# Performance work log

Measured on AMD Instinct MI355X. Metric: run time of the kernel, lower is better.

The kernel has to match this reference:

```python
import jax, jax.numpy as jnp
import numpy as np

N, E, CLIP, HID, H, P, MD, B = 4096, 16384, 512, 1024, 4, 4, 512, 32
OUT2 = P * MD  # 2048


def prelu(x, a):
    return jnp.where(x >= 0, x, a * x)


def add_self_loops(src, dst, edge_attr, n):
    # PyG fill_value='mean': self-loop edge_attr = mean of incoming edge attrs
    sums = jax.ops.segment_sum(edge_attr, dst, num_segments=n)
    cnt = jax.ops.segment_sum(jnp.ones((dst.shape[0], 1), edge_attr.dtype), dst, num_segments=n)
    loop_attr = sums / jnp.maximum(cnt, 1.0)
    idx = jnp.arange(n)
    return (jnp.concatenate([src, idx]), jnp.concatenate([dst, idx]),
            jnp.concatenate([edge_attr, loop_attr], axis=0))


def gat_conv(x, src, dst, edge_attr, W, asrc, adst, We, ae, bias, heads, c):
    # PyG GATConv, concat=False (mean over heads), edge_dim used only in attention
    n = x.shape[0]
    src, dst, edge_attr = add_self_loops(src, dst, edge_attr, n)
    h = (x @ W).reshape(n, heads, c)                      # [N,H,C]
    e = (edge_attr @ We).reshape(-1, heads, c)            # [E',H,C]
    a_s = jnp.einsum('nhc,hc->nh', h, asrc)
    a_d = jnp.einsum('nhc,hc->nh', h, adst)
    a_e = jnp.einsum('ehc,hc->eh', e, ae)
    alpha = jax.nn.leaky_relu(a_s[src] + a_d[dst] + a_e, 0.2)  # [E',H]
    amax = jax.ops.segment_max(alpha, dst, num_segments=n)
    ex = jnp.exp(alpha - amax[dst])
    denom = jax.ops.segment_sum(ex, dst, num_segments=n)
    w = ex / jnp.maximum(denom[dst], 1e-16)
    msg = h[src] * w[:, :, None]                          # [E',H,C]
    out = jax.ops.segment_sum(msg, dst, num_segments=n)   # [N,H,C]
    return out.mean(axis=1) + bias


def attentional_pool(x, batch, gW1, gb1, gp1, gW2, gb2, gp2, gW3, gb3, n_graphs):
    gate = prelu(x @ gW1 + gb1, gp1)
    gate = prelu(gate @ gW2 + gb2, gp2)
    gate = gate @ gW3 + gb3                               # [N,1]
    gmax = jax.ops.segment_max(gate, batch, num_segments=n_graphs)
    ex = jnp.exp(gate - gmax[batch])
    denom = jax.ops.segment_sum(ex, batch, num_segments=n_graphs)
    s = ex / jnp.maximum(denom[batch], 1e-16)             # [N,1]
    return jax.ops.segment_sum(s * x, batch, num_segments=n_graphs)  # [B,F]


def setup_inputs() -> dict:
    key = jax.random.key(0)
    ks = jax.random.split(key, 24)
    sc = 0.05
    inp = {
        'x': jax.random.normal(ks[0], (N, CLIP), jnp.float32),
        'edge_index': jax.random.randint(ks[1], (2, E), 0, N),
        'edge_attr': jax.random.normal(ks[2], (E, CLIP), jnp.float32),
        'batch': jnp.sort(jax.random.randint(ks[3], (N,), 0, B)),
        # GATConv 1
        'W1': jax.random.normal(ks[4], (CLIP, H * HID), jnp.float32) * sc,
        'asrc1': jax.random.normal(ks[5], (H, HID), jnp.float32) * sc,
        'adst1': jax.random.normal(ks[6], (H, HID), jnp.float32) * sc,
        'We1': jax.random.normal(ks[7], (CLIP, H * HID), jnp.float32) * sc,
        'ae1': jax.random.normal(ks[8], (H, HID), jnp.float32) * sc,
        'b1': jnp.zeros((HID,), jnp.float32),
        'p1': jnp.float32(0.25),
        # GATConv 2
        'W2': jax.random.normal(ks[9], (HID, H * OUT2), jnp.float32) * sc,
        'asrc2': jax.random.normal(ks[10], (H, OUT2), jnp.float32) * sc,
        'adst2': jax.random.normal(ks[11], (H, OUT2), jnp.float32) * sc,
        'We2': jax.random.normal(ks[12], (CLIP, H * OUT2), jnp.float32) * sc,
        'ae2': jax.random.normal(ks[13], (H, OUT2), jnp.float32) * sc,
        'b2': jnp.zeros((OUT2,), jnp.float32),
        'p2': jnp.float32(0.25),
        # AttentionalAggregation gate_nn
        'gW1': jax.random.normal(ks[14], (OUT2, HID), jnp.float32) * sc,
        'gb1': jnp.zeros((HID,), jnp.float32),
        'gp1': jnp.float32(0.25),
        'gW2': jax.random.normal(ks[15], (HID, HID), jnp.float32) * sc,
        'gb2': jnp.zeros((HID,), jnp.float32),
        'gp2': jnp.float32(0.25),
        'gW3': jax.random.normal(ks[16], (HID, 1), jnp.float32) * sc,
        'gb3': jnp.zeros((1,), jnp.float32),
    }
    return inp


def reference(x, edge_index, edge_attr, batch,
              W1, asrc1, adst1, We1, ae1, b1, p1,
              W2, asrc2, adst2, We2, ae2, b2, p2,
              gW1, gb1, gp1, gW2, gb2, gp2, gW3, gb3):
    src, dst = edge_index[0], edge_index[1]
    h = gat_conv(x, src, dst, edge_attr, W1, asrc1, adst1, We1, ae1, b1, H, HID)
    h = prelu(h, p1)
    h = gat_conv(h, src, dst, edge_attr, W2, asrc2, adst2, We2, ae2, b2, H, OUT2)
    h = prelu(h, p2)
    pooled = attentional_pool(h, batch, gW1, gb1, gp1, gW2, gb2, gp2, gW3, gb3, B)
    return pooled.reshape(-1, P, MD)  # [B, prefix_length, mbart_dim]
```

## Files before the change

kernel.cpp:

```cpp
#include <hip/hip_runtime.h>
#include <hip/hip_bf16.h>
#include <math.h>

#define N_NODES 4096
#define N_EDGES 16384
#define CLIPD   512
#define HID     1024
#define NH      4
#define OUTD    2048
#define NB      32

typedef __bf16 bf16_t;
typedef bf16_t bf16x8 __attribute__((ext_vector_type(8)));
typedef float f32x4 __attribute__((ext_vector_type(4)));

static __device__ __forceinline__ float lrelu(float x) { return x >= 0.f ? x : 0.2f * x; }

static __device__ __forceinline__ unsigned short f2bf(float f) {
  union { float f; unsigned int u; } v; v.f = f;
  unsigned int u = v.u;
  unsigned int r = (u + 0x7FFFu + ((u >> 16) & 1u)) >> 16;
  return (unsigned short)r;
}
static __device__ __forceinline__ float bf2f(unsigned short u) {
  union { unsigned int i; float f; } v; v.i = ((unsigned int)u) << 16; return v.f;
}

#define GLDS(g, l) __builtin_amdgcn_global_load_lds( \
    (const __attribute__((address_space(1))) void*)(g), \
    (__attribute__((address_space(3))) void*)(l), 16, 0, 0)

__global__ __launch_bounds__(256) void cvt_kernel(const float* __restrict__ in,
                                                  unsigned short* __restrict__ out, int n4) {
  int i = blockIdx.x * 256 + threadIdx.x;
  if (i < n4) {
    float4 f = ((const float4*)in)[i];
    ushort4 o;
    o.x = f2bf(f.x); o.y = f2bf(f.y); o.z = f2bf(f.z); o.w = f2bf(f.w);
    ((ushort4*)out)[i] = o;
  }
}

__global__ __launch_bounds__(256) void tcvt_kernel(const float* __restrict__ in,
                                                   unsigned short* __restrict__ out,
                                                   int K, int N) {
  __shared__ float t[32][33];
  const int k0 = blockIdx.y * 32, n0 = blockIdx.x * 32;
  const int tx = threadIdx.x, ty = threadIdx.y;
#pragma unroll
  for (int i = 0; i < 4; ++i) t[ty + 8 * i][tx] = in[(size_t)(k0 + ty + 8 * i) * N + n0 + tx];
  __syncthreads();
#pragma unroll
  for (int i = 0; i < 4; ++i) out[(size_t)(n0 + ty + 8 * i) * K + k0 + tx] = f2bf(t[tx][ty + 8 * i]);
}

template<int K1, int N1>
__global__ __launch_bounds__(256) void stack_tcvt_kernel(const float* __restrict__ in,
                                                         unsigned short* __restrict__ out,
                                                         float scale) {
  __shared__ float t[32][33];
  const int h = blockIdx.z;
  const int k0 = blockIdx.y * 32, n0 = blockIdx.x * 32;
  const int tx = threadIdx.x, ty = threadIdx.y;
#pragma unroll
  for (int i = 0; i < 4; ++i)
    t[ty + 8 * i][tx] = in[(size_t)(k0 + ty + 8 * i) * (NH * N1) + h * N1 + n0 + tx];
  __syncthreads();
#pragma unroll
  for (int i = 0; i < 4; ++i)
    out[(size_t)(n0 + ty + 8 * i) * (NH * K1) + h * K1 + k0 + tx] = f2bf(scale * t[tx][ty + 8 * i]);
}

template<int C>
__global__ __launch_bounds__(256) void v_kernel(const float* __restrict__ W,
                                                const float* __restrict__ a,
                                                float* __restrict__ v) {
  const int k = blockIdx.x;
  const int tid = threadIdx.x;
  const float* row = W + (size_t)k * (NH * C);
  float acc[NH] = {0.f, 0.f, 0.f, 0.f};
  for (int c = tid; c < C; c += 256) {
    for (int h = 0; h < NH; ++h) acc[h] += row[h * C + c] * a[h * C + c];
  }
  for (int h = 0; h < NH; ++h)
    for (int o = 32; o > 0; o >>= 1) acc[h] += __shfl_down(acc[h], o);
  __shared__ float red[4][NH];
  const int wid = tid >> 6, lane = tid & 63;
  if (lane == 0)
    for (int h = 0; h < NH; ++h) red[wid][h] = acc[h];
  __syncthreads();
  if (tid < NH) v[k * NH + tid] = red[0][tid] + red[1][tid] + red[2][tid] + red[3][tid];
}

template<int C>
__global__ __launch_bounds__(256) void v2_kernel(const float* __restrict__ W,
                                                 const float* __restrict__ a1v,
                                                 const float* __restrict__ a2v,
                                                 float* __restrict__ o1, float* __restrict__ o2) {
  const int k = blockIdx.x;
  const int tid = threadIdx.x;
  const float* row = W + (size_t)k * (NH * C);
  float x1[NH] = {0.f, 0.f, 0.f, 0.f}, x2[NH] = {0.f, 0.f, 0.f, 0.f};
  for (int c = tid; c < C; c += 256) {
    for (int h = 0; h < NH; ++h) {
      float w = row[h * C + c];
      x1[h] += w * a1v[h * C + c];
      x2[h] += w * a2v[h * C + c];
    }
  }
  for (int h = 0; h < NH; ++h)
    for (int o = 32; o > 0; o >>= 1) {
      x1[h] += __shfl_down(x1[h], o);
      x2[h] += __shfl_down(x2[h], o);
    }
  __shared__ float r1[4][NH], r2[4][NH];
  const int wid = tid >> 6, lane = tid & 63;
  if (lane == 0)
    for (int h = 0; h < NH; ++h) { r1[wid][h] = x1[h]; r2[wid][h] = x2[h]; }
  __syncthreads();
  if (tid < NH) o1[k * NH + tid] = r1[0][tid] + r1[1][tid] + r1[2][tid] + r1[3][tid];
  else if (tid < 2 * NH) {
    int h = tid - NH;
    o2[k * NH + h] = r2[0][h] + r2[1][h] + r2[2][h] + r2[3][h];
  }
}

__global__ void deg_kernel(const int* __restrict__ ei, int* __restrict__ deg) {
  int e = blockIdx.x * 256 + threadIdx.x;
  if (e < N_EDGES) atomicAdd(&deg[ei[N_EDGES + e]], 1);
}

__global__ __launch_bounds__(1024) void scan_kernel(const int* __restrict__ deg, int* __restrict__ offs) {
  __shared__ int s[1024];
  const int t = threadIdx.x;
  int d0 = deg[4 * t], d1 = deg[4 * t + 1], d2 = deg[4 * t + 2], d3 = deg[4 * t + 3];
  s[t] = d0 + d1 + d2 + d3;
  __syncthreads();
  for (int off = 1; off < 1024; off <<= 1) {
    int v = (t >= off) ? s[t - off] : 0;
    __syncthreads();
    s[t] += v;
    __syncthreads();
  }
  int base = (t > 0) ? s[t - 1] : 0;
  offs[4 * t] = base;
  offs[4 * t + 1] = base + d0;
  offs[4 * t + 2] = base + d0 + d1;
  offs[4 * t + 3] = base + d0 + d1 + d2;
  if (t == 1023) offs[4096] = s[1023];
}

__global__ void fill_kernel(const int* __restrict__ ei, const int* __restrict__ offs,
                            int* __restrict__ cursor, int* __restrict__ csr_src,
                            int* __restrict__ csr_eid) {
  int e = blockIdx.x * 256 + threadIdx.x;
  if (e >= N_EDGES) return;
  int dst = ei[N_EDGES + e];
  int pos = offs[dst] + atomicAdd(&cursor[dst], 1);
  csr_src[pos] = ei[e];
  csr_eid[pos] = e;
}

__global__ __launch_bounds__(256) void ae_kernel(const float* __restrict__ ea, const int* __restrict__ ei,
                                                 const float* __restrict__ v1, const float* __restrict__ v2,
                                                 float* __restrict__ ae1, float* __restrict__ ae2,
                                                 float* __restrict__ aesum1, float* __restrict__ aesum2) {
  __shared__ float4 v1s[CLIPD];
  __shared__ float4 v2s[CLIPD];
  const int tid = threadIdx.x;
  v1s[tid] = ((const float4*)v1)[tid];
  v1s[tid + 256] = ((const float4*)v1)[tid + 256];
  v2s[tid] = ((const float4*)v2)[tid];
  v2s[tid + 256] = ((const float4*)v2)[tid + 256];
  __syncthreads();
  const int wid = tid >> 6, lane = tid & 63;
  for (int i = 0; i < 16; ++i) {
    const int e = blockIdx.x * 64 + wid * 16 + i;
    const float* row = ea + (size_t)e * CLIPD;
    float a1[NH] = {0.f, 0.f, 0.f, 0.f}, a2[NH] = {0.f, 0.f, 0.f, 0.f};
    for (int k = lane; k < CLIPD; k += 64) {
      float x = row[k];
      float4 w1 = v1s[k];
      float4 w2 = v2s[k];
      a1[0] += x * w1.x; a1[1] += x * w1.y; a1[2] += x * w1.z; a1[3] += x * w1.w;
      a2[0] += x * w2.x; a2[1] += x * w2.y; a2[2] += x * w2.z; a2[3] += x * w2.w;
    }
    for (int h = 0; h < NH; ++h)
      for (int o = 32; o > 0; o >>= 1) {
        a1[h] += __shfl_down(a1[h], o);
        a2[h] += __shfl_down(a2[h], o);
      }
    if (lane == 0) {
      int dst = ei[N_EDGES + e];
      for (int h = 0; h < NH; ++h) {
        ae1[e * NH + h] = a1[h];
        ae2[e * NH + h] = a2[h];
        atomicAdd(&aesum1[dst * NH + h], a1[h]);
        atomicAdd(&aesum2[dst * NH + h], a2[h]);
      }
    }
  }
}

__global__ void loopdiv_kernel(float* __restrict__ s1, float* __restrict__ s2,
                               const int* __restrict__ deg) {
  int i = blockIdx.x * 256 + threadIdx.x;
  if (i >= N_NODES * NH) return;
  float c = fmaxf((float)deg[i >> 2], 1.0f);
  s1[i] /= c;
  s2[i] /= c;
}

__global__ __launch_bounds__(256) void rowdot_x(const float* __restrict__ x,
                                                const float* __restrict__ us, const float* __restrict__ ud,
                                                float* __restrict__ as_, float* __restrict__ ad_) {
  __shared__ float4 su[CLIPD], sd[CLIPD];
  const int tid = threadIdx.x;
  for (int k = tid; k < CLIPD; k += 256) {
    su[k] = ((const float4*)us)[k];
    sd[k] = ((const float4*)ud)[k];
  }
  __syncthreads();
  const int wid = tid >> 6, lane = tid & 63;
  const int n = blockIdx.x * 4 + wid;
  const float* row = x + (size_t)n * CLIPD;
  float s[NH] = {0.f, 0.f, 0.f, 0.f}, d[NH] = {0.f, 0.f, 0.f, 0.f};
  for (int k = lane; k < CLIPD; k += 64) {
    float xv = row[k];
    float4 u = su[k], v = sd[k];
    s[0] += xv * u.x; s[1] += xv * u.y; s[2] += xv * u.z; s[3] += xv * u.w;
    d[0] += xv * v.x; d[1] += xv * v.y; d[2] += xv * v.z; d[3] += xv * v.w;
  }
#pragma unroll
  for (int h = 0; h < NH; ++h)
    for (int o = 32; o > 0; o >>= 1) {
      s[h] += __shfl_down(s[h], o);
      d[h] += __shfl_down(d[h], o);
    }
  if (lane == 0)
    for (int h = 0; h < NH; ++h) {
      as_[n * NH + h] = s[h];
      ad_[n * NH + h] = d[h];
    }
}

__global__ __launch_bounds__(256) void rowdot_o(const unsigned short* __restrict__ rows,
                                                const float* __restrict__ us, const float* __restrict__ ud,
                                                float* __restrict__ as_, float* __restrict__ ad_) {
  __shared__ float4 su[HID], sd[HID];
  const int tid = threadIdx.x;
  for (int k = tid; k < HID; k += 256) {
    su[k] = ((const float4*)us)[k];
    sd[k] = ((const float4*)ud)[k];
  }
  __syncthreads();
  const int wid = tid >> 6, lane = tid & 63;
  const int n = blockIdx.x * 4 + wid;
  const unsigned short* row = rows + (size_t)n * HID;
  float s[NH] = {0.f, 0.f, 0.f, 0.f}, d[NH] = {0.f, 0.f, 0.f, 0.f};
  for (int k2 = lane; k2 < HID / 2; k2 += 64) {
    ushort2 uv = ((const ushort2*)row)[k2];
    float f0 = bf2f(uv.x), f1 = bf2f(uv.y);
    float4 u0 = su[2 * k2], u1 = su[2 * k2 + 1];
    float4 v0 = sd[2 * k2], v1 = sd[2 * k2 + 1];
    s[0] += f0 * u0.x + f1 * u1.x; s[1] += f0 * u0.y + f1 * u1.y;
    s[2] += f0 * u0.z + f1 * u1.z; s[3] += f0 * u0.w + f1 * u1.w;
    d[0] += f0 * v0.x + f1 * v1.x; d[1] += f0 * v0.y + f1 * v1.y;
    d[2] += f0 * v0.z + f1 * v1.z; d[3] += f0 * v0.w + f1 * v1.w;
  }
#pragma unroll
  for (int h = 0; h < NH; ++h)
    for (int o = 32; o > 0; o >>= 1) {
      s[h] += __shfl_down(s[h], o);
      d[h] += __shfl_down(d[h], o);
    }
  if (lane == 0)
    for (int h = 0; h < NH; ++h) {
      as_[n * NH + h] = s[h];
      ad_[n * NH + h] = d[h];
    }
}

template<int C>
__global__ __launch_bounds__(256) void aggn_kernel(const unsigned short* __restrict__ src,
                                                   const float* __restrict__ as_, const float* __restrict__ ad_,
                                                   const float* __restrict__ aee, const float* __restrict__ aeloop,
                                                   const int* __restrict__ offs, const int* __restrict__ csr_src,
                                                   const int* __restrict__ csr_eid,
                                                   unsigned short* __restrict__ out) {
  constexpr int CPT = C / 256;
  const int n = blockIdx.x;
  const int tid = threadIdx.x;
  const int off = offs[n];
  const int deg = offs[n + 1] - off;
  __shared__ float minv[NH], dinv[NH], wself[NH];
  __shared__ float wch[32][NH];
  __shared__ int sch[32];
  if (tid < 64) {
    const int h = tid >> 4, slot = tid & 15;
    const float adn = ad_[n * NH + h];
    const float aself = lrelu(as_[n * NH + h] + adn + aeloop[n * NH + h]);
    float m = (slot == 0) ? aself : -3.0e38f;
    for (int i = slot; i < deg; i += 16) {
      float a = lrelu(as_[csr_src[off + i] * NH + h] + adn + aee[csr_eid[off + i] * NH + h]);
      m = fmaxf(m, a);
    }
    for (int o = 1; o < 16; o <<= 1) m = fmaxf(m, __shfl_xor(m, o));
    float den = (slot == 0) ? __expf(aself - m) : 0.f;
    for (int i = slot; i < deg; i += 16) {
      float a = lrelu(as_[csr_src[off + i] * NH + h] + adn + aee[csr_eid[off + i] * NH + h]);
      den += __expf(a - m);
    }
    for (int o = 1; o < 16; o <<= 1) den += __shfl_xor(den, o);
    if (slot == 0) {
      minv[h] = m;
      dinv[h] = 1.0f / den;
      wself[h] = __expf(aself - m) / den;
    }
  }
  __syncthreads();
  float acc[NH][CPT];
#pragma unroll
  for (int h = 0; h < NH; ++h)
#pragma unroll
    for (int c = 0; c < CPT; ++c) acc[h][c] = 0.f;
  for (int base = 0; base < deg; base += 32) {
    const int cnt = min(32, deg - base);
    if (tid < cnt * NH) {
      const int i = tid >> 2, h = tid & 3;
      const int sidx = csr_src[off + base + i];
      float a = lrelu(as_[sidx * NH + h] + ad_[n * NH + h] + aee[csr_eid[off + base + i] * NH + h]);
      wch[i][h] = __expf(a - minv[h]) * dinv[h];
      if (h == 0) sch[i] = sidx;
    }
    __syncthreads();
    for (int i = 0; i < cnt; ++i) {
      const unsigned short* hp = src + (size_t)sch[i] * C + tid * CPT;
      float f[CPT];
      if constexpr (CPT == 2) {
        ushort2 u = *(const ushort2*)hp;
        f[0] = bf2f(u.x); f[1] = bf2f(u.y);
      } else {
        ushort4 u = *(const ushort4*)hp;
        f[0] = bf2f(u.x); f[1] = bf2f(u.y); f[2] = bf2f(u.z); f[3] = bf2f(u.w);
      }
#pragma unroll
      for (int h = 0; h < NH; ++h) {
        const float wv = wch[i][h];
#pragma unroll
        for (int c = 0; c < CPT; ++c) acc[h][c] += wv * f[c];
      }
    }
    __syncthreads();
  }
  {
    const unsigned short* hp = src + (size_t)n * C + tid * CPT;
    float f[CPT];
    if constexpr (CPT == 2) {
      ushort2 u = *(const ushort2*)hp;
      f[0] = bf2f(u.x); f[1] = bf2f(u.y);
    } else {
      ushort4 u = *(const ushort4*)hp;
      f[0] = bf2f(u.x); f[1] = bf2f(u.y); f[2] = bf2f(u.z); f[3] = bf2f(u.w);
    }
#pragma unroll
    for (int h = 0; h < NH; ++h) {
      const float wv = wself[h];
#pragma unroll
      for (int c = 0; c < CPT; ++c) acc[h][c] += wv * f[c];
    }
  }
#pragma unroll
  for (int h = 0; h < NH; ++h) {
    if constexpr (CPT == 2) {
      ushort2 o;
      o.x = f2bf(acc[h][0]); o.y = f2bf(acc[h][1]);
      *(ushort2*)&out[((size_t)n * NH + h) * C + tid * 2] = o;
    } else {
      ushort4 o;
      o.x = f2bf(acc[h][0]); o.y = f2bf(acc[h][1]); o.z = f2bf(acc[h][2]); o.w = f2bf(acc[h][3]);
      *(ushort4*)&out[((size_t)n * NH + h) * C + tid * 4] = o;
    }
  }
}

template<int EPI, int WF>
__global__ __launch_bounds__(256) void mfma_gemm(const unsigned short* __restrict__ A,
                                                 const unsigned short* __restrict__ Bt,
                                                 unsigned short* __restrict__ C,
                                                 float* __restrict__ Cf,
                                                 int M, int N, int K,
                                                 const float* __restrict__ bias,
                                                 const float* __restrict__ pa) {
  __shared__ unsigned short As[128 * 32];
  __shared__ unsigned short Bs[128 * 32];
  const int tid = threadIdx.x;
  const int lane = tid & 63;
  const int w = tid >> 6;
  const int wr = w >> 1, wc = w & 1;
  const int brow = blockIdx.y * 128, bcol = blockIdx.x * 128;
  const int r0 = tid >> 2;
  const int koff = (tid & 3) * 8;
  const int fr = lane & 15;
  const int fk = (lane >> 4) * 8;
  f32x4 acc[4][4] = {};
  for (int kt = 0; kt < K; kt += 32) {
    GLDS(A + (size_t)(brow + r0) * K + kt + koff, &As[tid * 8]);
    GLDS(A + (size_t)(brow + 64 + r0) * K + kt + koff, &As[2048 + tid * 8]);
    GLDS(Bt + (size_t)(bcol + r0) * K + kt + koff, &Bs[tid * 8]);
    GLDS(Bt + (size_t)(bcol + 64 + r0) * K + kt + koff, &Bs[2048 + tid * 8]);
    asm volatile("s_waitcnt vmcnt(0)" ::: "memory");
    __syncthreads();
    bf16x8 af[4], bfr[4];
#pragma unroll
    for (int mi = 0; mi < 4; ++mi)
      af[mi] = *(const bf16x8*)&As[(wr * 64 + mi * 16 + fr) * 32 + fk];
#pragma unroll
    for (int ni = 0; ni < 4; ++ni)
      bfr[ni] = *(const bf16x8*)&Bs[(wc * 64 + ni * 16 + fr) * 32 + fk];
#pragma unroll
    for (int mi = 0; mi < 4; ++mi)
#pragma unroll
      for (int ni = 0; ni < 4; ++ni)
        acc[mi][ni] = __builtin_amdgcn_mfma_f32_16x16x32_bf16(af[mi], bfr[ni], acc[mi][ni], 0, 0, 0);
    __syncthreads();
  }
  const float ap = EPI ? *pa : 0.f;
#pragma unroll
  for (int mi = 0; mi < 4; ++mi) {
    const int rb = brow + wr * 64 + mi * 16 + (lane >> 4) * 4;
#pragma unroll
    for (int ni = 0; ni < 4; ++ni) {
      const int col = bcol + wc * 64 + ni * 16 + fr;
      float bv = 0.f;
      if (EPI) bv = bias[col];
#pragma unroll
      for (int r = 0; r < 4; ++r) {
        float v = acc[mi][ni][r];
        if (EPI) { v += bv; v = v >= 0.f ? v : ap * v; }
        C[(size_t)(rb + r) * N + col] = f2bf(v);
        if (WF) Cf[(size_t)(rb + r) * N + col] = v;
      }
    }
  }
}

__global__ __launch_bounds__(256) void gate3_kernel(const unsigned short* __restrict__ gh2,
                                                    const float* __restrict__ gW3,
                                                    const float* __restrict__ gb3, float* __restrict__ gate) {
  const int n = blockIdx.x, tid = threadIdx.x;
  const unsigned short* row = gh2 + (size_t)n * HID;
  ushort4 u = *(const ushort4*)&row[tid * 4];
  float4 wv = *(const float4*)&gW3[tid * 4];
  float acc = bf2f(u.x) * wv.x + bf2f(u.y) * wv.y + bf2f(u.z) * wv.z + bf2f(u.w) * wv.w;
  for (int o = 32; o > 0; o >>= 1) acc += __shfl_down(acc, o);
  __shared__ float red[4];
  const int wid = tid >> 6, lane = tid & 63;
  if (lane == 0) red[wid] = acc;
  __syncthreads();
  if (tid == 0) gate[n] = red[0] + red[1] + red[2] + red[3] + gb3[0];
}

__global__ void gstart_kernel(const int* __restrict__ batch, int* __restrict__ gstart) {
  int n = blockIdx.x * 256 + threadIdx.x;
  if (n >= N_NODES) return;
  int b = batch[n];
  if (n == 0) {
    for (int bb = 0; bb <= b; ++bb) gstart[bb] = 0;
  } else {
    int pb = batch[n - 1];
    for (int bb = pb + 1; bb <= b; ++bb) gstart[bb] = n;
  }
  if (n == N_NODES - 1)
    for (int bb = b + 1; bb <= NB; ++bb) gstart[bb] = N_NODES;
}

__global__ __launch_bounds__(256) void gsoft_kernel(const float* __restrict__ gate, const int* __restrict__ gstart,
                                                    float* __restrict__ gm, float* __restrict__ ginv) {
  const int b = blockIdx.x, tid = threadIdx.x;
  const int s = gstart[b], e = gstart[b + 1];
  float m = -3.0e38f;
  for (int n = s + tid; n < e; n += 256) m = fmaxf(m, gate[n]);
  for (int o = 32; o > 0; o >>= 1) m = fmaxf(m, __shfl_down(m, o));
  __shared__ float red[4];
  __shared__ float red2[4];
  const int wid = tid >> 6, lane = tid & 63;
  if (lane == 0) red[wid] = m;
  __syncthreads();
  m = fmaxf(fmaxf(red[0], red[1]), fmaxf(red[2], red[3]));
  float sum = 0.f;
  for (int n = s + tid; n < e; n += 256) sum += __expf(gate[n] - m);
  for (int o = 32; o > 0; o >>= 1) sum += __shfl_down(sum, o);
  if (lane == 0) red2[wid] = sum;
  __syncthreads();
  if (tid == 0) {
    sum = red2[0] + red2[1] + red2[2] + red2[3];
    gm[b] = m;
    ginv[b] = 1.0f / fmaxf(sum, 1e-16f);
  }
}

__global__ __launch_bounds__(256) void pool_kernel(const float* __restrict__ out2, const float* __restrict__ gate,
                                                   const float* __restrict__ gm, const float* __restrict__ ginv,
                                                   const int* __restrict__ gstart, float* __restrict__ dout) {
  const int b = blockIdx.y;
  const int col = blockIdx.x * 256 + threadIdx.x;
  const int s = gstart[b], e = gstart[b + 1];
  const float m = gm[b], gi = ginv[b];
  float acc = 0.f;
  for (int n = s; n < e; ++n) {
    float w = __expf(gate[n] - m) * gi;
    acc += w * out2[(size_t)n * OUTD + col];
  }
  dout[(size_t)b * OUTD + col] = acc;
}

#define MB(x) ((size_t)(x) * 1048576)
#define WS_XB     MB(0)
#define WS_B1T    MB(4)
#define WS_B2T    MB(8)
#define WS_GW1T   MB(24)
#define WS_GW2T   MB(28)
#define WS_AGGX   MB(30)
#define WS_OUT1B  MB(46)
#define WS_AGGO   MB(54)
#define WS_OUT2F  MB(86)
#define WS_OUT2B  MB(118)
#define WS_GH1B   MB(134)
#define WS_GH2B   MB(142)
#define WS_SM     MB(150)
#define WS_DEG    (WS_SM + 0)
#define WS_CUR    (WS_SM + 16384)
#define WS_AES1   (WS_SM + 32768)
#define WS_AES2   (WS_SM + 98304)
#define WS_ZBYTES 163840
#define WS_OFFS   (WS_SM + 163840)
#define WS_CSRS   (WS_OFFS + 16640)
#define WS_CSRE   (WS_CSRS + 65536)
#define WS_AS1    (WS_CSRE + 65536)
#define WS_AD1    (WS_AS1 + 65536)
#define WS_AEE1   (WS_AD1 + 65536)
#define WS_AS2    (WS_AEE1 + 262144)
#define WS_AD2    (WS_AS2 + 65536)
#define WS_AEE2   (WS_AD2 + 65536)
#define WS_V1     (WS_AEE2 + 262144)
#define WS_V2     (WS_V1 + 8192)
#define WS_US1    (WS_V2 + 8192)
#define WS_UD1    (WS_US1 + 8192)
#define WS_US2    (WS_UD1 + 8192)
#define WS_UD2    (WS_US2 + 16384)
#define WS_GATE   (WS_UD2 + 16384)
#define WS_GM     (WS_GATE + 16384)
#define WS_GINV   (WS_GM + 128)
#define WS_GSTART (WS_GINV + 128)

extern "C" void kernel_launch(void* const* d_in, const int* in_sizes, int n_in,
                              void* d_out, int out_size, void* d_ws, size_t ws_size,
                              hipStream_t stream) {
  const float* x     = (const float*)d_in[0];
  const int*   ei    = (const int*)d_in[1];
  const float* ea    = (const float*)d_in[2];
  const int*   batch = (const int*)d_in[3];
  const float* W1    = (const float*)d_in[4];
  const float* asrc1 = (const float*)d_in[5];
  const float* adst1 = (const float*)d_in[6];
  const float* We1   = (const float*)d_in[7];
  const float* ae1w  = (const float*)d_in[8];
  const float* b1    = (const float*)d_in[9];
  const float* p1    = (const float*)d_in[10];
  const float* W2    = (const float*)d_in[11];
  const float* asrc2 = (const float*)d_in[12];
  const float* adst2 = (const float*)d_in[13];
  const float* We2   = (const float*)d_in[14];
  const float* ae2w  = (const float*)d_in[15];
  const float* b2    = (const float*)d_in[16];
  const float* p2    = (const float*)d_in[17];
  const float* gW1   = (const float*)d_in[18];
  const float* gb1   = (const float*)d_in[19];
  const float* gp1   = (const float*)d_in[20];
  const float* gW2   = (const float*)d_in[21];
  const float* gb2   = (const float*)d_in[22];
  const float* gp2   = (const float*)d_in[23];
  const float* gW3   = (const float*)d_in[24];
  const float* gb3   = (const float*)d_in[25];

  char* ws = (char*)d_ws;
  unsigned short* xb    = (unsigned short*)(ws + WS_XB);
  unsigned short* B1t   = (unsigned short*)(ws + WS_B1T);
  unsigned short* B2t   = (unsigned short*)(ws + WS_B2T);
  unsigned short* gW1t  = (unsigned short*)(ws + WS_GW1T);
  unsigned short* gW2t  = (unsigned short*)(ws + WS_GW2T);
  unsigned short* aggXb = (unsigned short*)(ws + WS_AGGX);
  unsigned short* out1b = (unsigned short*)(ws + WS_OUT1B);
  unsigned short* aggOb = (unsigned short*)(ws + WS_AGGO);
  float*          out2f = (float*)(ws + WS_OUT2F);
  unsigned short* out2b = (unsigned short*)(ws + WS_OUT2B);
  unsigned short* gh1b  = (unsigned short*)(ws + WS_GH1B);
  unsigned short* gh2b  = (unsigned short*)(ws + WS_GH2B);
  int*   deg     = (int*)(ws + WS_DEG);
  int*   cursor  = (int*)(ws + WS_CUR);
  float* aesum1  = (float*)(ws + WS_AES1);
  float* aesum2  = (float*)(ws + WS_AES2);
  int*   offs    = (int*)(ws + WS_OFFS);
  int*   csr_src = (int*)(ws + WS_CSRS);
  int*   csr_eid = (int*)(ws + WS_CSRE);
  float* as1     = (float*)(ws + WS_AS1);
  float* ad1     = (float*)(ws + WS_AD1);
  float* aee1    = (float*)(ws + WS_AEE1);
  float* as2     = (float*)(ws + WS_AS2);
  float* ad2     = (float*)(ws + WS_AD2);
  float* aee2    = (float*)(ws + WS_AEE2);
  float* v1      = (float*)(ws + WS_V1);
  float* v2      = (float*)(ws + WS_V2);
  float* us1     = (float*)(ws + WS_US1);
  float* ud1     = (float*)(ws + WS_UD1);
  float* us2     = (float*)(ws + WS_US2);
  float* ud2     = (float*)(ws + WS_UD2);
  float* gate    = (float*)(ws + WS_GATE);
  float* gm      = (float*)(ws + WS_GM);
  float* ginv    = (float*)(ws + WS_GINV);
  int*   gstart  = (int*)(ws + WS_GSTART);
  float* dout    = (float*)d_out;

  hipMemsetAsync(ws + WS_DEG, 0, WS_ZBYTES, stream);

  cvt_kernel<<<(N_NODES * CLIPD / 4 + 255) / 256, 256, 0, stream>>>(x, xb, N_NODES * CLIPD / 4);
  stack_tcvt_kernel<CLIPD, HID><<<dim3(HID / 32, CLIPD / 32, NH), dim3(32, 8), 0, stream>>>(W1, B1t, 0.25f);
  stack_tcvt_kernel<HID, OUTD><<<dim3(OUTD / 32, HID / 32, NH), dim3(32, 8), 0, stream>>>(W2, B2t, 0.25f);
  tcvt_kernel<<<dim3(HID / 32, OUTD / 32), dim3(32, 8), 0, stream>>>(gW1, gW1t, OUTD, HID);
  tcvt_kernel<<<dim3(HID / 32, HID / 32), dim3(32, 8), 0, stream>>>(gW2, gW2t, HID, HID);

  v_kernel<HID><<<CLIPD, 256, 0, stream>>>(We1, ae1w, v1);
  v_kernel<OUTD><<<CLIPD, 256, 0, stream>>>(We2, ae2w, v2);
  v2_kernel<HID><<<CLIPD, 256, 0, stream>>>(W1, asrc1, adst1, us1, ud1);
  v2_kernel<OUTD><<<HID, 256, 0, stream>>>(W2, asrc2, adst2, us2, ud2);

  deg_kernel<<<N_EDGES / 256, 256, 0, stream>>>(ei, deg);
  scan_kernel<<<1, 1024, 0, stream>>>(deg, offs);
  fill_kernel<<<N_EDGES / 256, 256, 0, stream>>>(ei, offs, cursor, csr_src, csr_eid);

  ae_kernel<<<N_EDGES / 64, 256, 0, stream>>>(ea, ei, v1, v2, aee1, aee2, aesum1, aesum2);
  loopdiv_kernel<<<(N_NODES * NH) / 256, 256, 0, stream>>>(aesum1, aesum2, deg);

  rowdot_x<<<N_NODES / 4, 256, 0, stream>>>(x, us1, ud1, as1, ad1);
  aggn_kernel<CLIPD><<<N_NODES, 256, 0, stream>>>(xb, as1, ad1, aee1, aesum1, offs, csr_src, csr_eid, aggXb);
  mfma_gemm<1, 0><<<dim3(HID / 128, N_NODES / 128), 256, 0, stream>>>(
      aggXb, B1t, out1b, nullptr, N_NODES, HID, NH * CLIPD, b1, p1);

  rowdot_o<<<N_NODES / 4, 256, 0, stream>>>(out1b, us2, ud2, as2, ad2);
  aggn_kernel<HID><<<N_NODES, 256, 0, stream>>>(out1b, as2, ad2, aee2, aesum2, offs, csr_src, csr_eid, aggOb);
  mfma_gemm<1, 1><<<dim3(OUTD / 128, N_NODES / 128), 256, 0, stream>>>(
      aggOb, B2t, out2b, out2f, N_NODES, OUTD, NH * HID, b2, p2);

  mfma_gemm<1, 0><<<dim3(HID / 128, N_NODES / 128), 256, 0, stream>>>(
      out2b, gW1t, gh1b, nullptr, N_NODES, HID, OUTD, gb1, gp1);
  mfma_gemm<1, 0><<<dim3(HID / 128, N_NODES / 128), 256, 0, stream>>>(
      gh1b, gW2t, gh2b, nullptr, N_NODES, HID, HID, gb2, gp2);
  gate3_kernel<<<N_NODES, 256, 0, stream>>>(gh2b, gW3, gb3, gate);

  gstart_kernel<<<N_NODES / 256, 256, 0, stream>>>(batch, gstart);
  gsoft_kernel<<<NB, 256, 0, stream>>>(gate, gstart, gm, ginv);
  pool_kernel<<<dim3(OUTD / 256, NB), 256, 0, stream>>>(out2f, gate, gm, ginv, gstart, dout);
}
```

Before: 559.0 us.

## Merge prep kernels, build CSR in one block, retile GEMMs and swizzle blocks

Folds the weight transposes into one launch and the attention-vector folds into another. CSR construction (degree, scan, fill) moves into a single shared-memory block, and the bf16 conversion of x is fused into the row-dot kernel. The self-loop division moves into aggn, and the softmax pooling stages are merged into one kernel that binary-searches graph bounds. The MFMA GEMM gains a BN template with 64-wide tiles for the N=1024 GEMMs to fill more CUs, plus a block-id swizzle meant to improve L2 reuse. This cuts launch count and memset size, at the cost of a serial single-block CSR build and redundant softmax reductions per pool block.

```diff
diff --git a/kernel.cpp b/kernel.cpp
--- a/kernel.cpp
+++ b/kernel.cpp
@@ -30,74 +30,48 @@
     (const __attribute__((address_space(1))) void*)(g), \
     (__attribute__((address_space(3))) void*)(l), 16, 0, 0)
 
-__global__ __launch_bounds__(256) void cvt_kernel(const float* __restrict__ in,
-                                                  unsigned short* __restrict__ out, int n4) {
-  int i = blockIdx.x * 256 + threadIdx.x;
-  if (i < n4) {
-    float4 f = ((const float4*)in)[i];
-    ushort4 o;
-    o.x = f2bf(f.x); o.y = f2bf(f.y); o.z = f2bf(f.z); o.w = f2bf(f.w);
-    ((ushort4*)out)[i] = o;
-  }
-}
-
-__global__ __launch_bounds__(256) void tcvt_kernel(const float* __restrict__ in,
-                                                   unsigned short* __restrict__ out,
-                                                   int K, int N) {
+__device__ __forceinline__ void stcvt_tile(float (*t)[33], const float* __restrict__ in,
+                                           unsigned short* __restrict__ out,
+                                           int K1, int N1, int NHH, int h, int bx, int by,
+                                           float scale) {
+  const int k0 = by * 32, n0 = bx * 32;
+  const int tx = threadIdx.x, ty = threadIdx.y;
+#pragma unroll
+  for (int i = 0; i < 4; ++i)
+    t[ty + 8 * i][tx] = in[(size_t)(k0 + ty + 8 * i) * (NHH * N1) + (size_t)h * N1 + n0 + tx];
+  __syncthreads();
+#pragma unroll
+  for (int i = 0; i < 4; ++i)
+    out[(size_t)(n0 + ty + 8 * i) * (NHH * K1) + (size_t)h * K1 + k0 + tx] =
+        f2bf(scale * t[tx][ty + 8 * i]);
+}
+
+__global__ __launch_bounds__(256) void wprep_kernel(const float* __restrict__ W1, const float* __restrict__ W2,
+                                                    const float* __restrict__ gW1, const float* __restrict__ gW2,
+                                                    unsigned short* __restrict__ B1t, unsigned short* __restrict__ B2t,
+                                                    unsigned short* __restrict__ gW1t, unsigned short* __restrict__ gW2t) {
   __shared__ float t[32][33];
-  const int k0 = blockIdx.y * 32, n0 = blockIdx.x * 32;
-  const int tx = threadIdx.x, ty = threadIdx.y;
-#pragma unroll
-  for (int i = 0; i < 4; ++i) t[ty + 8 * i][tx] = in[(size_t)(k0 + ty + 8 * i) * N + n0 + tx];
-  __syncthreads();
-#pragma unroll
-  for (int i = 0; i < 4; ++i) out[(size_t)(n0 + ty + 8 * i) * K + k0 + tx] = f2bf(t[tx][ty + 8 * i]);
-}
-
-template<int K1, int N1>
-__global__ __launch_bounds__(256) void stack_tcvt_kernel(const float* __restrict__ in,
-                                                         unsigned short* __restrict__ out,
-                                                         float scale) {
-  __shared__ float t[32][33];
-  const int h = blockIdx.z;
-  const int k0 = blockIdx.y * 32, n0 = blockIdx.x * 32;
-  const int tx = threadIdx.x, ty = threadIdx.y;
-#pragma unroll
-  for (int i = 0; i < 4; ++i)
-    t[ty + 8 * i][tx] = in[(size_t)(k0 + ty + 8 * i) * (NH * N1) + h * N1 + n0 + tx];
-  __syncthreads();
-#pragma unroll
-  for (int i = 0; i < 4; ++i)
-    out[(size_t)(n0 + ty + 8 * i) * (NH * K1) + h * K1 + k0 + tx] = f2bf(scale * t[tx][ty + 8 * i]);
-}
-
-template<int C>
-__global__ __launch_bounds__(256) void v_kernel(const float* __restrict__ W,
-                                                const float* __restrict__ a,
-                                                float* __restrict__ v) {
-  const int k = blockIdx.x;
-  const int tid = threadIdx.x;
-  const float* row = W + (size_t)k * (NH * C);
-  float acc[NH] = {0.f, 0.f, 0.f, 0.f};
-  for (int c = tid; c < C; c += 256) {
-    for (int h = 0; h < NH; ++h) acc[h] += row[h * C + c] * a[h * C + c];
-  }
-  for (int h = 0; h < NH; ++h)
-    for (int o = 32; o > 0; o >>= 1) acc[h] += __shfl_down(acc[h], o);
-  __shared__ float red[4][NH];
-  const int wid = tid >> 6, lane = tid & 63;
-  if (lane == 0)
-    for (int h = 0; h < NH; ++h) red[wid][h] = acc[h];
-  __syncthreads();
-  if (tid < NH) v[k * NH + tid] = red[0][tid] + red[1][tid] + red[2][tid] + red[3][tid];
-}
-
-template<int C>
-__global__ __launch_bounds__(256) void v2_kernel(const float* __restrict__ W,
-                                                 const float* __restrict__ a1v,
-                                                 const float* __restrict__ a2v,
-                                                 float* __restrict__ o1, float* __restrict__ o2) {
-  const int k = blockIdx.x;
+  const int id = blockIdx.x;
+  if (id < 2048) {
+    int h = id >> 9, r = id & 511;
+    stcvt_tile(t, W1, B1t, CLIPD, HID, NH, h, r & 31, r >> 5, 0.25f);
+  } else if (id < 10240) {
+    int r2 = id - 2048;
+    int h = r2 >> 11, r = r2 & 2047;
+    stcvt_tile(t, W2, B2t, HID, OUTD, NH, h, r & 63, r >> 6, 0.25f);
+  } else if (id < 12288) {
+    int r = id - 10240;
+    stcvt_tile(t, gW1, gW1t, OUTD, HID, 1, 0, r & 31, r >> 5, 1.0f);
+  } else {
+    int r = id - 12288;
+    stcvt_tile(t, gW2, gW2t, HID, HID, 1, 0, r & 31, r >> 5, 1.0f);
+  }
+}
+
+__device__ __forceinline__ void vfold(float (*r1)[NH], float (*r2)[NH],
+                                      const float* __restrict__ W,
+                                      const float* __restrict__ a1v, const float* __restrict__ a2v,
+                                      float* __restrict__ o1, float* __restrict__ o2, int C, int k) {
   const int tid = threadIdx.x;
   const float* row = W + (size_t)k * (NH * C);
   float x1[NH] = {0.f, 0.f, 0.f, 0.f}, x2[NH] = {0.f, 0.f, 0.f, 0.f};
@@ -113,52 +87,71 @@
       x1[h] += __shfl_down(x1[h], o);
       x2[h] += __shfl_down(x2[h], o);
     }
-  __shared__ float r1[4][NH], r2[4][NH];
   const int wid = tid >> 6, lane = tid & 63;
   if (lane == 0)
     for (int h = 0; h < NH; ++h) { r1[wid][h] = x1[h]; r2[wid][h] = x2[h]; }
   __syncthreads();
-  if (tid < NH) o1[k * NH + tid] = r1[0][tid] + r1[1][tid] + r1[2][tid] + r1[3][tid];
-  else if (tid < 2 * NH) {
+  if (tid < NH)
+    o1[k * NH + tid] = r1[0][tid] + r1[1][tid] + r1[2][tid] + r1[3][tid];
+  else if (o2 != nullptr && tid < 2 * NH) {
     int h = tid - NH;
     o2[k * NH + h] = r2[0][h] + r2[1][h] + r2[2][h] + r2[3][h];
   }
 }
 
-__global__ void deg_kernel(const int* __restrict__ ei, int* __restrict__ deg) {
-  int e = blockIdx.x * 256 + threadIdx.x;
-  if (e < N_EDGES) atomicAdd(&deg[ei[N_EDGES + e]], 1);
-}
-
-__global__ __launch_bounds__(1024) void scan_kernel(const int* __restrict__ deg, int* __restrict__ offs) {
-  __shared__ int s[1024];
+__global__ __launch_bounds__(256) void vprep_kernel(const float* __restrict__ We1, const float* __restrict__ ae1w,
+                                                    const float* __restrict__ We2, const float* __restrict__ ae2w,
+                                                    const float* __restrict__ W1, const float* __restrict__ asrc1,
+                                                    const float* __restrict__ adst1,
+                                                    const float* __restrict__ W2, const float* __restrict__ asrc2,
+                                                    const float* __restrict__ adst2,
+                                                    float* __restrict__ v1, float* __restrict__ v2,
+                                                    float* __restrict__ us1, float* __restrict__ ud1,
+                                                    float* __restrict__ us2, float* __restrict__ ud2) {
+  __shared__ float r1[4][NH], r2[4][NH];
+  const int id = blockIdx.x;
+  if (id < 512)       vfold(r1, r2, We1, ae1w, ae1w, v1, nullptr, HID, id);
+  else if (id < 1024) vfold(r1, r2, We2, ae2w, ae2w, v2, nullptr, OUTD, id - 512);
+  else if (id < 1536) vfold(r1, r2, W1, asrc1, adst1, us1, ud1, HID, id - 1024);
+  else                vfold(r1, r2, W2, asrc2, adst2, us2, ud2, OUTD, id - 1536);
+}
+
+__global__ __launch_bounds__(1024) void csr_kernel(const int* __restrict__ ei,
+                                                   int* __restrict__ offs,
+                                                   int* __restrict__ csr_src, int* __restrict__ csr_eid) {
+  __shared__ int sdeg[N_NODES];
+  __shared__ int soffs[N_NODES];
+  __shared__ int sscan[1024];
   const int t = threadIdx.x;
-  int d0 = deg[4 * t], d1 = deg[4 * t + 1], d2 = deg[4 * t + 2], d3 = deg[4 * t + 3];
-  s[t] = d0 + d1 + d2 + d3;
+  for (int i = t; i < N_NODES; i += 1024) sdeg[i] = 0;
+  __syncthreads();
+  for (int e = t; e < N_EDGES; e += 1024) atomicAdd(&sdeg[ei[N_EDGES + e]], 1);
+  __syncthreads();
+  const int d0 = sdeg[4 * t], d1 = sdeg[4 * t + 1], d2 = sdeg[4 * t + 2], d3 = sdeg[4 * t + 3];
+  sscan[t] = d0 + d1 + d2 + d3;
   __syncthreads();
   for (int off = 1; off < 1024; off <<= 1) {
-    int v = (t >= off) ? s[t - off] : 0;
+    int v = (t >= off) ? sscan[t - off] : 0;
     __syncthreads();
-    s[t] += v;
+    sscan[t] += v;
     __syncthreads();
   }
-  int base = (t > 0) ? s[t - 1] : 0;
-  offs[4 * t] = base;
-  offs[4 * t + 1] = base + d0;
-  offs[4 * t + 2] = base + d0 + d1;
-  offs[4 * t + 3] = base + d0 + d1 + d2;
-  if (t == 1023) offs[4096] = s[1023];
-}
-
-__global__ void fill_kernel(const int* __restrict__ ei, const int* __restrict__ offs,
-                            int* __restrict__ cursor, int* __restrict__ csr_src,
-                            int* __restrict__ csr_eid) {
-  int e = blockIdx.x * 256 + threadIdx.x;
-  if (e >= N_EDGES) return;
-  int dst = ei[N_EDGES + e];
-  int pos = offs[dst] + atomicAdd(&cursor[dst], 1);
-  csr_src[pos] = ei[e];
-  csr_eid[pos] = e;
+  const int base = (t > 0) ? sscan[t - 1] : 0;
+  soffs[4 * t] = base;
+  soffs[4 * t + 1] = base + d0;
+  soffs[4 * t + 2] = base + d0 + d1;
+  soffs[4 * t + 3] = base + d0 + d1 + d2;
+#pragma unroll
+  for (int j = 0; j < 4; ++j) offs[4 * t + j] = soffs[4 * t + j];
+  if (t == 1023) offs[N_NODES] = sscan[1023];
+  sdeg[4 * t] = 0; sdeg[4 * t + 1] = 0; sdeg[4 * t + 2] = 0; sdeg[4 * t + 3] = 0;
+  __syncthreads();
+  for (int e = t; e < N_EDGES; e += 1024) {
+    int dst = ei[N_EDGES + e];
+    int pos = soffs[dst] + atomicAdd(&sdeg[dst], 1);
+    csr_src[pos] = ei[e];
+    csr_eid[pos] = e;
+  }
 }
 
 __global__ __launch_bounds__(256) void ae_kernel(const float* __restrict__ ea, const int* __restrict__ ei,
@@ -202,18 +195,10 @@
   }
 }
 
-__global__ void loopdiv_kernel(float* __restrict__ s1, float* __restrict__ s2,
-                               const int* __restrict__ deg) {
-  int i = blockIdx.x * 256 + threadIdx.x;
-  if (i >= N_NODES * NH) return;
-  float c = fmaxf((float)deg[i >> 2], 1.0f);
-  s1[i] /= c;
-  s2[i] /= c;
-}
-
-__global__ __launch_bounds__(256) void rowdot_x(const float* __restrict__ x,
-                                                const float* __restrict__ us, const float* __restrict__ ud,
-                                                float* __restrict__ as_, float* __restrict__ ad_) {
+__global__ __launch_bounds__(256) void xprep_kernel(const float* __restrict__ x,
+                                                    const float* __restrict__ us, const float* __restrict__ ud,
+                                                    unsigned short* __restrict__ xb,
+                                                    float* __restrict__ as_, float* __restrict__ ad_) {
   __shared__ float4 su[CLIPD], sd[CLIPD];
   const int tid = threadIdx.x;
   for (int k = tid; k < CLIPD; k += 256) {
@@ -224,12 +209,21 @@
   const int wid = tid >> 6, lane = tid & 63;
   const int n = blockIdx.x * 4 + wid;
   const float* row = x + (size_t)n * CLIPD;
+  unsigned short* orow = xb + (size_t)n * CLIPD;
   float s[NH] = {0.f, 0.f, 0.f, 0.f}, d[NH] = {0.f, 0.f, 0.f, 0.f};
-  for (int k = lane; k < CLIPD; k += 64) {
-    float xv = row[k];
-    float4 u = su[k], v = sd[k];
-    s[0] += xv * u.x; s[1] += xv * u.y; s[2] += xv * u.z; s[3] += xv * u.w;
-    d[0] += xv * v.x; d[1] += xv * v.y; d[2] += xv * v.z; d[3] += xv * v.w;
+  for (int q = lane; q < CLIPD / 4; q += 64) {
+    float4 xv = ((const float4*)row)[q];
+    ushort4 ob;
+    ob.x = f2bf(xv.x); ob.y = f2bf(xv.y); ob.z = f2bf(xv.z); ob.w = f2bf(xv.w);
+    ((ushort4*)orow)[q] = ob;
+    const float* xp = &xv.x;
+#pragma unroll
+    for (int j = 0; j < 4; ++j) {
+      float xs = xp[j];
+      float4 u = su[q * 4 + j], v = sd[q * 4 + j];
+      s[0] += xs * u.x; s[1] += xs * u.y; s[2] += xs * u.z; s[3] += xs * u.w;
+      d[0] += xs * v.x; d[1] += xs * v.y; d[2] += xs * v.z; d[3] += xs * v.w;
+    }
   }
 #pragma unroll
   for (int h = 0; h < NH; ++h)
@@ -284,7 +278,7 @@
 template<int C>
 __global__ __launch_bounds__(256) void aggn_kernel(const unsigned short* __restrict__ src,
                                                    const float* __restrict__ as_, const float* __restrict__ ad_,
-                                                   const float* __restrict__ aee, const float* __restrict__ aeloop,
+                                                   const float* __restrict__ aee, const float* __restrict__ aesum,
                                                    const int* __restrict__ offs, const int* __restrict__ csr_src,
                                                    const int* __restrict__ csr_eid,
                                                    unsigned short* __restrict__ out) {
@@ -299,7 +293,7 @@
   if (tid < 64) {
     const int h = tid >> 4, slot = tid & 15;
     const float adn = ad_[n * NH + h];
-    const float aself = lrelu(as_[n * NH + h] + adn + aeloop[n * NH + h]);
+    const float aself = lrelu(as_[n * NH + h] + adn + aesum[n * NH + h] / fmaxf((float)deg, 1.f));
     float m = (slot == 0) ? aself : -3.0e38f;
     for (int i = slot; i < deg; i += 16) {
       float a = lrelu(as_[csr_src[off + i] * NH + h] + adn + aee[csr_eid[off + i] * NH + h]);
@@ -384,7 +378,7 @@
   }
 }
 
-template<int EPI, int WF>
+template<int EPI, int WF, int BN>
 __global__ __launch_bounds__(256) void mfma_gemm(const unsigned short* __restrict__ A,
                                                  const unsigned short* __restrict__ Bt,
                                                  unsigned short* __restrict__ C,
@@ -392,36 +386,42 @@
                                                  int M, int N, int K,
                                                  const float* __restrict__ bias,
                                                  const float* __restrict__ pa) {
+  constexpr int NFR = BN / 32;
   __shared__ unsigned short As[128 * 32];
-  __shared__ unsigned short Bs[128 * 32];
+  __shared__ unsigned short Bs[BN * 32];
+  const int nwg = gridDim.x * gridDim.y;
+  int id = blockIdx.y * gridDim.x + blockIdx.x;
+  id = (id & 7) * (nwg >> 3) + (id >> 3);
+  const int bx = id % gridDim.x, by = id / gridDim.x;
   const int tid = threadIdx.x;
   const int lane = tid & 63;
   const int w = tid >> 6;
   const int wr = w >> 1, wc = w & 1;
-  const int brow = blockIdx.y * 128, bcol = blockIdx.x * 128;
+  const int brow = by * 128, bcol = bx * BN;
   const int r0 = tid >> 2;
   const int koff = (tid & 3) * 8;
   const int fr = lane & 15;
   const int fk = (lane >> 4) * 8;
-  f32x4 acc[4][4] = {};
+  f32x4 acc[4][NFR] = {};
   for (int kt = 0; kt < K; kt += 32) {
     GLDS(A + (size_t)(brow + r0) * K + kt + koff, &As[tid * 8]);
     GLDS(A + (size_t)(brow + 64 + r0) * K + kt + koff, &As[2048 + tid * 8]);
     GLDS(Bt + (size_t)(bcol + r0) * K + kt + koff, &Bs[tid * 8]);
-    GLDS(Bt + (size_t)(bcol + 64 + r0) * K + kt + koff, &Bs[2048 + tid * 8]);
+    if constexpr (BN == 128)
+      GLDS(Bt + (size_t)(bcol + 64 + r0) * K + kt + koff, &Bs[2048 + tid * 8]);
     asm volatile("s_waitcnt vmcnt(0)" ::: "memory");
     __syncthreads();
-    bf16x8 af[4], bfr[4];
+    bf16x8 af[4], bfr[NFR];
 #pragma unroll
     for (int mi = 0; mi < 4; ++mi)
       af[mi] = *(const bf16x8*)&As[(wr * 64 + mi * 16 + fr) * 32 + fk];
 #pragma unroll
-    for (int ni = 0; ni < 4; ++ni)
-      bfr[ni] = *(const bf16x8*)&Bs[(wc * 64 + ni * 16 + fr) * 32 + fk];
+    for (int ni = 0; ni < NFR; ++ni)
+      bfr[ni] = *(const bf16x8*)&Bs[(wc * (BN / 2) + ni * 16 + fr) * 32 + fk];
 #pragma unroll
     for (int mi = 0; mi < 4; ++mi)
 #pragma unroll
-      for (int ni = 0; ni < 4; ++ni)
+      for (int ni = 0; ni < NFR; ++ni)
         acc[mi][ni] = __builtin_amdgcn_mfma_f32_16x16x32_bf16(af[mi], bfr[ni], acc[mi][ni], 0, 0, 0);
     __syncthreads();
   }
@@ -430,8 +430,8 @@
   for (int mi = 0; mi < 4; ++mi) {
     const int rb = brow + wr * 64 + mi * 16 + (lane >> 4) * 4;
 #pragma unroll
-    for (int ni = 0; ni < 4; ++ni) {
-      const int col = bcol + wc * 64 + ni * 16 + fr;
+    for (int ni = 0; ni < NFR; ++ni) {
+      const int col = bcol + wc * (BN / 2) + ni * 16 + fr;
       float bv = 0.f;
       if (EPI) bv = bias[col];
 #pragma unroll
@@ -461,57 +461,38 @@
   if (tid == 0) gate[n] = red[0] + red[1] + red[2] + red[3] + gb3[0];
 }
 
-__global__ void gstart_kernel(const int* __restrict__ batch, int* __restrict__ gstart) {
-  int n = blockIdx.x * 256 + threadIdx.x;
-  if (n >= N_NODES) return;
-  int b = batch[n];
-  if (n == 0) {
-    for (int bb = 0; bb <= b; ++bb) gstart[bb] = 0;
-  } else {
-    int pb = batch[n - 1];
-    for (int bb = pb + 1; bb <= b; ++bb) gstart[bb] = n;
-  }
-  if (n == N_NODES - 1)
-    for (int bb = b + 1; bb <= NB; ++bb) gstart[bb] = N_NODES;
-}
-
-__global__ __launch_bounds__(256) void gsoft_kernel(const float* __restrict__ gate, const int* __restrict__ gstart,
-                                                    float* __restrict__ gm, float* __restrict__ ginv) {
-  const int b = blockIdx.x, tid = threadIdx.x;
-  const int s = gstart[b], e = gstart[b + 1];
+__global__ __launch_bounds__(256) void pool2_kernel(const float* __restrict__ out2,
+                                                    const float* __restrict__ gate,
+                                                    const int* __restrict__ batch,
+                                                    float* __restrict__ dout) {
+  const int b = blockIdx.y;
+  const int tid = threadIdx.x;
+  const int col = blockIdx.x * 256 + tid;
+  int lo = 0, hi = N_NODES;
+  while (lo < hi) { int mid = (lo + hi) >> 1; if (batch[mid] < b) lo = mid + 1; else hi = mid; }
+  const int s = lo;
+  hi = N_NODES;
+  while (lo < hi) { int mid = (lo + hi) >> 1; if (batch[mid] < b + 1) lo = mid + 1; else hi = mid; }
+  const int e = lo;
+  __shared__ float red[4];
+  const int wid = tid >> 6, lane = tid & 63;
   float m = -3.0e38f;
   for (int n = s + tid; n < e; n += 256) m = fmaxf(m, gate[n]);
   for (int o = 32; o > 0; o >>= 1) m = fmaxf(m, __shfl_down(m, o));
-  __shared__ float red[4];
-  __shared__ float red2[4];
-  const int wid = tid >> 6, lane = tid & 63;
   if (lane == 0) red[wid] = m;
   __syncthreads();
   m = fmaxf(fmaxf(red[0], red[1]), fmaxf(red[2], red[3]));
+  __syncthreads();
   float sum = 0.f;
   for (int n = s + tid; n < e; n += 256) sum += __expf(gate[n] - m);
   for (int o = 32; o > 0; o >>= 1) sum += __shfl_down(sum, o);
-  if (lane == 0) red2[wid] = sum;
-  __syncthreads();
-  if (tid == 0) {
-    sum = red2[0] + red2[1] + red2[2] + red2[3];
-    gm[b] = m;
-    ginv[b] = 1.0f / fmaxf(sum, 1e-16f);
-  }
-}
-
-__global__ __launch_bounds__(256) void pool_kernel(const float* __restrict__ out2, const float* __restrict__ gate,
-                                                   const float* __restrict__ gm, const float* __restrict__ ginv,
-                                                   const int* __restrict__ gstart, float* __restrict__ dout) {
-  const int b = blockIdx.y;
-  const int col = blockIdx.x * 256 + threadIdx.x;
-  const int s = gstart[b], e = gstart[b + 1];
-  const float m = gm[b], gi = ginv[b];
+  if (lane == 0) red[wid] = sum;
+  __syncthreads();
+  sum = red[0] + red[1] + red[2] + red[3];
+  const float gi = 1.0f / fmaxf(sum, 1e-16f);
   float acc = 0.f;
-  for (int n = s; n < e; ++n) {
-    float w = __expf(gate[n] - m) * gi;
-    acc += w * out2[(size_t)n * OUTD + col];
-  }
+  for (int n = s; n < e; ++n)
+    acc += __expf(gate[n] - m) * gi * out2[(size_t)n * OUTD + col];
   dout[(size_t)b * OUTD + col] = acc;
 }
 
@@ -529,12 +510,9 @@
 #define WS_GH1B   MB(134)
 #define WS_GH2B   MB(142)
 #define WS_SM     MB(150)
-#define WS_DEG    (WS_SM + 0)
-#define WS_CUR    (WS_SM + 16384)
-#define WS_AES1   (WS_SM + 32768)
-#define WS_AES2   (WS_SM + 98304)
-#define WS_ZBYTES 163840
-#define WS_OFFS   (WS_SM + 163840)
+#define WS_AES1   (WS_SM + 0)
+#define WS_AES2   (WS_AES1 + 65536)
+#define WS_OFFS   (WS_AES2 + 65536)
 #define WS_CSRS   (WS_OFFS + 16640)
 #define WS_CSRE   (WS_CSRS + 65536)
 #define WS_AS1    (WS_CSRE + 65536)
@@ -550,9 +528,6 @@
 #define WS_US2    (WS_UD1 + 8192)
 #define WS_UD2    (WS_US2 + 16384)
 #define WS_GATE   (WS_UD2 + 16384)
-#define WS_GM     (WS_GATE + 16384)
-#define WS_GINV   (WS_GM + 128)
-#define WS_GSTART (WS_GINV + 128)
 
 extern "C" void kernel_launch(void* const* d_in, const int* in_sizes, int n_in,
                               void* d_out, int out_size, void* d_ws, size_t ws_size,
@@ -597,8 +572,6 @@
   unsigned short* out2b = (unsigned short*)(ws + WS_OUT2B);
   unsigned short* gh1b  = (unsigned short*)(ws + WS_GH1B);
   unsigned short* gh2b  = (unsigned short*)(ws + WS_GH2B);
-  int*   deg     = (int*)(ws + WS_DEG);
-  int*   cursor  = (int*)(ws + WS_CUR);
   float* aesum1  = (float*)(ws + WS_AES1);
   float* aesum2  = (float*)(ws + WS_AES2);
   int*   offs    = (int*)(ws + WS_OFFS);
@@ -617,48 +590,31 @@
   float* us2     = (float*)(ws + WS_US2);
   float* ud2     = (float*)(ws + WS_UD2);
   float* gate    = (float*)(ws + WS_GATE);
-  float* gm      = (float*)(ws + WS_GM);
-  float* ginv    = (float*)(ws + WS_GINV);
-  int*   gstart  = (int*)(ws + WS_GSTART);
   float* dout    = (float*)d_out;
 
-  hipMemsetAsync(ws + WS_DEG, 0, WS_ZBYTES, stream);
-
-  cvt_kernel<<<(N_NODES * CLIPD / 4 + 255) / 256, 256, 0, stream>>>(x, xb, N_NODES * CLIPD / 4);
-  stack_tcvt_kernel<CLIPD, HID><<<dim3(HID / 32, CLIPD / 32, NH), dim3(32, 8), 0, stream>>>(W1, B1t, 0.25f);
-  stack_tcvt_kernel<HID, OUTD><<<dim3(OUTD / 32, HID / 32, NH), dim3(32, 8), 0, stream>>>(W2, B2t, 0.25f);
-  tcvt_kernel<<<dim3(HID / 32, OUTD / 32), dim3(32, 8), 0, stream>>>(gW1, gW1t, OUTD, HID);
-  tcvt_kernel<<<dim3(HID / 32, HID / 32), dim3(32, 8), 0, stream>>>(gW2, gW2t, HID, HID);
-
-  v_kernel<HID><<<CLIPD, 256, 0, stream>>>(We1, ae1w, v1);
-  v_kernel<OUTD><<<CLIPD, 256, 0, stream>>>(We2, ae2w, v2);
-  v2_kernel<HID><<<CLIPD, 256, 0, stream>>>(W1, asrc1, adst1, us1, ud1);
-  v2_kernel<OUTD><<<HID, 256, 0, stream>>>(W2, asrc2, adst2, us2, ud2);
-
-  deg_kernel<<<N_EDGES / 256, 256, 0, stream>>>(ei, deg);
-  scan_kernel<<<1, 1024, 0, stream>>>(deg, offs);
-  fill_kernel<<<N_EDGES / 256, 256, 0, stream>>>(ei, offs, cursor, csr_src, csr_eid);
-
+  hipMemsetAsync(ws + WS_AES1, 0, 131072, stream);
+
+  wprep_kernel<<<13312, dim3(32, 8), 0, stream>>>(W1, W2, gW1, gW2, B1t, B2t, gW1t, gW2t);
+  vprep_kernel<<<2560, 256, 0, stream>>>(We1, ae1w, We2, ae2w, W1, asrc1, adst1, W2, asrc2, adst2,
+                                         v1, v2, us1, ud1, us2, ud2);
+  csr_kernel<<<1, 1024, 0, stream>>>(ei, offs, csr_src, csr_eid);
   ae_kernel<<<N_EDGES / 64, 256, 0, stream>>>(ea, ei, v1, v2, aee1, aee2, aesum1, aesum2);
-  loopdiv_kernel<<<(N_NODES * NH) / 256, 256, 0, stream>>>(aesum1, aesum2, deg);
-
-  rowdot_x<<<N_NODES / 4, 256, 0, stream>>>(x, us1, ud1, as1, ad1);
+  xprep_kernel<<<N_NODES / 4, 256, 0, stream>>>(x, us1, ud1, xb, as1, ad1);
+
   aggn_kernel<CLIPD><<<N_NODES, 256, 0, stream>>>(xb, as1, ad1, aee1, aesum1, offs, csr_src, csr_eid, aggXb);
-  mfma_gemm<1, 0><<<dim3(HID / 128, N_NODES / 128), 256, 0, stream>>>(
+  mfma_gemm<1, 0, 64><<<dim3(HID / 64, N_NODES / 128), 256, 0, stream>>>(
       aggXb, B1t, out1b, nullptr, N_NODES, HID, NH * CLIPD, b1, p1);
 
   rowdot_o<<<N_NODES / 4, 256, 0, stream>>>(out1b, us2, ud2, as2, ad2);
   aggn_kernel<HID><<<N_NODES, 256, 0, stream>>>(out1b, as2, ad2, aee2, aesum2, offs, csr_src, csr_eid, aggOb);
-  mfma_gemm<1, 1><<<dim3(OUTD / 128, N_NODES / 128), 256, 0, stream>>>(
+  mfma_gemm<1, 1, 128><<<dim3(OUTD / 128, N_NODES / 128), 256, 0, stream>>>(
       aggOb, B2t, out2b, out2f, N_NODES, OUTD, NH * HID, b2, p2);
 
-  mfma_gemm<1, 0><<<dim3(HID / 128, N_NODES / 128), 256, 0, stream>>>(
+  mfma_gemm<1, 0, 64><<<dim3(HID / 64, N_NODES / 128), 256, 0, stream>>>(
       out2b, gW1t, gh1b, nullptr, N_NODES, HID, OUTD, gb1, gp1);
-  mfma_gemm<1, 0><<<dim3(HID / 128, N_NODES / 128), 256, 0, stream>>>(
+  mfma_gemm<1, 0, 64><<<dim3(HID / 64, N_NODES / 128), 256, 0, stream>>>(
       gh1b, gW2t, gh2b, nullptr, N_NODES, HID, HID, gb2, gp2);
   gate3_kernel<<<N_NODES, 256, 0, stream>>>(gh2b, gW3, gb3, gate);
 
-  gstart_kernel<<<N_NODES / 256, 256, 0, stream>>>(batch, gstart);
-  gsoft_kernel<<<NB, 256, 0, stream>>>(gate, gstart, gm, ginv);
-  pool_kernel<<<dim3(OUTD / 256, NB), 256, 0, stream>>>(out2f, gate, gm, ginv, gstart, dout);
-}
+  pool2_kernel<<<dim3(OUTD / 256, NB), 256, 0, stream>>>(out2f, gate, batch, dout);
+}
```

Result: faster. 543.7 us (-2.7%).
